# Kernel tuning notes

Hardware: AMD Instinct MI355X
Metric: run time of the kernel (lower is better)

## Reference

```python
import jax, jax.numpy as jnp
import numpy as np

NUM_QRYS = 300
NUM_CLASSES = 80
NUM_PAIRS = 4_000_000
NMS_CANDIDATES = 1000
NMS_THR = 0.65
MAX_SEGS = 100
REFINED_WEIGHT = 2.0
FH = FW = 256  # final mask grid resolution


def setup_inputs() -> dict:
    key = jax.random.key(0)
    k1, k2, k3, k4, k5, k6, k7 = jax.random.split(key, 7)
    cls_logits = jax.random.normal(k1, (NUM_QRYS, NUM_CLASSES + 1), jnp.float32)
    # valid xyxy boxes in normalized [0,1] coords
    b = jax.random.uniform(k2, (NUM_QRYS, 4), jnp.float32)
    x1 = b[:, 0] * 0.7
    y1 = b[:, 1] * 0.7
    x2 = x1 + 0.05 + b[:, 2] * 0.25
    y2 = y1 + 0.05 + b[:, 3] * 0.25
    pred_boxes = jnp.stack([x1, y1, x2, y2], axis=1)
    seg_logits = jax.random.normal(k3, (NUM_PAIRS,), jnp.float32)
    key_xy = jax.random.uniform(k4, (NUM_PAIRS, 2), jnp.float32)
    qry_ids = jax.random.randint(k5, (NUM_PAIRS,), 0, NUM_QRYS, jnp.int32)
    refined_mask = jax.random.randint(k6, (NUM_PAIRS,), 0, 2, jnp.int32).astype(bool)
    map_ids = jax.random.randint(k7, (NUM_PAIRS,), 0, 4, jnp.int32)
    return {"cls_logits": cls_logits, "pred_boxes": pred_boxes, "seg_logits": seg_logits,
            "key_xy": key_xy, "qry_ids": qry_ids, "refined_mask": refined_mask, "map_ids": map_ids}


def _box_iou(boxes):  # boxes: [C,4] xyxy -> [C,C]
    x1 = jnp.maximum(boxes[:, None, 0], boxes[None, :, 0])
    y1 = jnp.maximum(boxes[:, None, 1], boxes[None, :, 1])
    x2 = jnp.minimum(boxes[:, None, 2], boxes[None, :, 2])
    y2 = jnp.minimum(boxes[:, None, 3], boxes[None, :, 3])
    inter = jnp.clip(x2 - x1, 0.0) * jnp.clip(y2 - y1, 0.0)
    area = (boxes[:, 2] - boxes[:, 0]) * (boxes[:, 3] - boxes[:, 1])
    union = area[:, None] + area[None, :] - inter
    return inter / jnp.maximum(union, 1e-9)


def _nms_keep(iou, thr):
    # greedy NMS over score-sorted candidates (rows already in descending score order)
    C = iou.shape[0]
    idx = jnp.arange(C)
    def body(i, keep):
        sup = (iou[i] > thr) & (idx > i) & keep[i]
        return keep & ~sup
    return jax.lax.fori_loop(0, C, body, jnp.ones(C, dtype=bool))


def reference(cls_logits, pred_boxes, seg_logits, key_xy, qry_ids, refined_mask, map_ids):
    num_qrys = cls_logits.shape[0]
    # expand per-query class scores -> flat predictions (batch_size = 1)
    scores = jax.nn.sigmoid(cls_logits[:, :-1]).reshape(-1)          # [Q*C]
    feat_ids = jnp.repeat(jnp.arange(num_qrys), NUM_CLASSES)          # [Q*C]
    labels = jnp.tile(jnp.arange(NUM_CLASSES), num_qrys)              # [Q*C]
    # top-k candidates before NMS
    top_scores, cand = jax.lax.top_k(scores, NMS_CANDIDATES)
    cand_feats = feat_ids[cand]
    cand_labels = labels[cand]
    # class-aware (batched) NMS: offset boxes per label so classes don't suppress each other
    offs = cand_labels.astype(pred_boxes.dtype)[:, None] * 4.0
    cand_boxes = pred_boxes[cand_feats] + offs
    keep = _nms_keep(_box_iou(cand_boxes), NMS_THR)
    kept_scores = jnp.where(keep, top_scores, -jnp.inf)
    sel_scores, sel = jax.lax.top_k(kept_scores, MAX_SEGS)
    sel_scores = jnp.where(jnp.isfinite(sel_scores), sel_scores, 0.0)
    sel_feats = cand_feats[sel]
    # assemble per-query mask logit maps from sparse query-key pairs (scatter-max)
    px = jnp.clip((key_xy[:, 0] * FW).astype(jnp.int32), 0, FW - 1)
    py = jnp.clip((key_xy[:, 1] * FH).astype(jnp.int32), 0, FH - 1)
    w_logits = jnp.where(refined_mask, REFINED_WEIGHT * seg_logits, seg_logits)
    flat = qry_ids * (FH * FW) + py * FW + px                          # [num_pairs]
    qry_maps = jnp.full((num_qrys * FH * FW,), -1e4, cls_logits.dtype).at[flat].max(w_logits)
    qry_maps = qry_maps.reshape(num_qrys, FH, FW)
    mask_probs = jax.nn.sigmoid(qry_maps[sel_feats])                   # [MAX_SEGS, FH, FW]
    # score-weighted soft masks (float output; thresholding at mask_thr yields bool masks)
    return sel_scores[:, None, None] * mask_probs
```

## Files before the change

### kernel.cpp

```cpp
#include <hip/hip_runtime.h>

#define NQ        300
#define NC        80
#define NE        24000
#define CAND      1000
#define KSEL      100
#define NPAIRS    4000000
#define HB        4096
#define FHW       65536
#define NMS_THR_F 0.65f
#define MAPS_INIT 0x39E3BFFFu
#define INIT_VEC4 1638400

__device__ __forceinline__ unsigned enc_f32(float f) {
    unsigned u = __float_as_uint(f);
    return (u & 0x80000000u) ? ~u : (u | 0x80000000u);
}
__device__ __forceinline__ float dec_f32(unsigned k) {
    unsigned u = (k & 0x80000000u) ? (k ^ 0x80000000u) : ~k;
    return __uint_as_float(u);
}

__global__ __launch_bounds__(1024) void k_front(
    const float* __restrict__ cls,
    const float* __restrict__ pboxes,
    const unsigned* __restrict__ refined_raw,
    uint4* __restrict__ maps4,
    float* __restrict__ sel_score_g, int* __restrict__ sel_slot_g,
    int* __restrict__ qry2slot_g, unsigned* __restrict__ mode_flag_g)
{
    if (blockIdx.x > 0) {
        uint4 v; v.x = v.y = v.z = v.w = MAPS_INIT;
        for (int i = (int)(blockIdx.x - 1) * 1024 + (int)threadIdx.x;
             i < INIT_VEC4; i += 256 * 1024)
            maps4[i] = v;
        return;
    }

    __shared__ unsigned long long sbuf[4096];
    __shared__ float sbx[CAND], sby[CAND], sbz[CAND], sbw[CAND];
    __shared__ float sscore[CAND];
    __shared__ short sfeat[CAND];
    __shared__ unsigned char slab[CAND];
    __shared__ unsigned char skeep[CAND];
    __shared__ int wlist[16][64];
    __shared__ int q2s[NQ];
    __shared__ float ss[KSEL]; __shared__ int sf[KSEL];
    __shared__ unsigned subhist[64];
    __shared__ unsigned smode;
    __shared__ int sB, sT, sAbove, sCount, sN;

    unsigned* hist = (unsigned*)sbuf;
    int tid = threadIdx.x;
    int lane = tid & 63, wv = tid >> 6;

    for (int b = tid; b < HB; b += 1024) hist[b] = 0u;
    if (tid < 64) subhist[tid] = 0u;
    if (tid == 0) { smode = 0u; sCount = 0; }
    __syncthreads();

    unsigned long long lk[24];
    #pragma unroll
    for (int k = 0; k < 24; k++) {
        int e = tid + (k << 10);
        if (e < NE) {
            int q = e / NC, c = e - q * NC;
            float x = cls[q * (NC + 1) + c];
            float s = 1.f / (1.f + expf(-x));
            unsigned bits = __float_as_uint(s);
            lk[k] = ((unsigned long long)bits << 32) | (unsigned)(0xFFFFFFFFu - (unsigned)e);
            atomicAdd(&hist[bits >> 18], 1u);
        }
    }
    if (refined_raw[tid] > 1u) atomicOr(&smode, 1u);
    __syncthreads();

    if (tid == 0) {
        int acc = 0, B = 0;
        for (int b = HB - 1; b >= 0; b--) {
            acc += (int)hist[b];
            if (acc >= CAND) { B = b; break; }
        }
        sB = B; sAbove = acc - (int)hist[B];
    }
    __syncthreads();
    unsigned B = (unsigned)sB;

    #pragma unroll
    for (int k = 0; k < 24; k++) {
        int e = tid + (k << 10);
        if (e < NE && (unsigned)(lk[k] >> 50) == B)
            atomicAdd(&subhist[(unsigned)(lk[k] >> 44) & 63u], 1u);
    }
    __syncthreads();
    if (tid == 0) {
        int acc2 = sAbove, T = 0;
        for (int t = 63; t >= 0; t--) {
            acc2 += (int)subhist[t];
            if (acc2 >= CAND) { T = t; break; }
        }
        sT = T; sN = acc2;
    }
    __syncthreads();
    unsigned T = (unsigned)sT;

    #pragma unroll
    for (int k = 0; k < 24; k++) {
        int e = tid + (k << 10);
        if (e < NE) {
            unsigned long long key = lk[k];
            unsigned bkt = (unsigned)(key >> 50);
            unsigned sub = (unsigned)(key >> 44) & 63u;
            if (bkt > B || (bkt == B && sub >= T)) {
                int pos = atomicAdd(&sCount, 1);
                if (pos < 4096) sbuf[pos] = key;
            }
        }
    }
    __syncthreads();
    int n = min(sN, 4096);

    if (n <= 1024) {
        unsigned long long r = (tid < n) ? sbuf[tid] : 0ULL;
        for (int k = 2; k <= 1024; k <<= 1) {
            for (int j = k >> 1; j > 0; j >>= 1) {
                unsigned long long p;
                if (j >= 64) {
                    sbuf[tid] = r; __syncthreads();
                    p = sbuf[tid ^ j]; __syncthreads();
                } else {
                    p = __shfl_xor(r, j, 64);
                }
                bool d = (tid & k) != 0, lower = (tid & j) == 0;
                r = (d != lower) ? (r > p ? r : p) : (r < p ? r : p);
            }
        }
        sbuf[tid] = r;
        __syncthreads();
    } else {
        int nsort = 2048; while (nsort < n) nsort <<= 1;
        for (int i = n + tid; i < nsort; i += 1024) sbuf[i] = 0ULL;
        __syncthreads();
        for (int k = 2; k <= nsort; k <<= 1)
            for (int j = k >> 1; j > 0; j >>= 1) {
                for (int i = tid; i < nsort; i += 1024) {
                    int ixj = i ^ j;
                    if (ixj > i) {
                        unsigned long long a = sbuf[i], b2 = sbuf[ixj];
                        bool up = ((i & k) == 0);
                        if (up ? (a < b2) : (a > b2)) { sbuf[i] = b2; sbuf[ixj] = a; }
                    }
                }
                __syncthreads();
            }
    }

    if (tid < CAND) {
        unsigned long long key = sbuf[tid];
        unsigned bits = (unsigned)(key >> 32);
        unsigned e = 0xFFFFFFFFu - (unsigned)(key & 0xFFFFFFFFu);
        int feat = (int)e / NC, lab = (int)e - feat * NC;
        sscore[tid] = __uint_as_float(bits);
        sfeat[tid]  = (short)feat;
        slab[tid]   = (unsigned char)lab;
        float off = 4.f * (float)lab;
        const float4 pb = ((const float4*)pboxes)[feat];
        sbx[tid] = pb.x + off; sby[tid] = pb.y + off;
        sbz[tid] = pb.z + off; sbw[tid] = pb.w + off;
    }
    __syncthreads();

    for (int li = 0; li < 5; li++) {
        int lab = wv + (li << 4);
        int nb = 0;
        for (int c = 0; c < CAND; c += 64) {
            int i = c + lane;
            bool m = (i < CAND) && ((int)slab[i] == lab);
            unsigned long long bal = __ballot(m);
            if (m) {
                int r = nb + __popcll(bal & ((1ULL << lane) - 1ULL));
                if (r < 64) wlist[wv][r] = i;
            }
            nb += __popcll(bal);
        }
        int nl = min(nb, 64);
        __syncthreads();

        bool alive = lane < nl;
        float bxv = 0.f, byv = 0.f, bzv = 0.f, bwv = 0.f, ar = 0.f;
        int idx = -1;
        if (alive) {
            idx = wlist[wv][lane];
            bxv = sbx[idx]; byv = sby[idx]; bzv = sbz[idx]; bwv = sbw[idx];
            ar = (bzv - bxv) * (bwv - byv);
        }
        bool keep = alive;
        for (int i = 0; i < nl; i++) {
            float bix = __shfl(bxv, i), biy = __shfl(byv, i);
            float biz = __shfl(bzv, i), biw = __shfl(bwv, i);
            float ai  = __shfl(ar, i);
            int   ki  = __shfl((int)keep, i);
            if (ki && keep && lane > i) {
                float xx1 = fmaxf(bix, bxv), yy1 = fmaxf(biy, byv);
                float xx2 = fminf(biz, bzv), yy2 = fminf(biw, bwv);
                float inter = fmaxf(xx2 - xx1, 0.f) * fmaxf(yy2 - yy1, 0.f);
                float uni = ai + ar - inter;
                if (inter / fmaxf(uni, 1e-9f) > NMS_THR_F) keep = false;
            }
        }
        if (alive) skeep[idx] = keep ? 1 : 0;
    }
    __syncthreads();

    for (int q = tid; q < NQ; q += 1024) q2s[q] = -1;
    __syncthreads();
    if (tid < 64) {
        int base = 0;
        for (int c = 0; c < CAND; c += 64) {
            int i = c + lane;
            bool k = (i < CAND) && skeep[i];
            unsigned long long bal = __ballot(k);
            int pos = base + __popcll(bal & ((1ULL << lane) - 1ULL));
            if (k && pos < KSEL) { ss[pos] = sscore[i]; sf[pos] = (int)sfeat[i]; }
            base += __popcll(bal);
        }
        if (tid == 0) {
            int nsel = min(base, KSEL), nslots = 0;
            for (int s = 0; s < KSEL; s++) {
                if (s < nsel) {
                    int f = sf[s];
                    int sl = q2s[f];
                    if (sl < 0) { sl = nslots++; q2s[f] = sl; }
                    sel_slot_g[s] = sl; sel_score_g[s] = ss[s];
                } else {
                    sel_slot_g[s] = -1; sel_score_g[s] = 0.f;
                }
            }
            *mode_flag_g = smode;
        }
    }
    __syncthreads();
    for (int q = tid; q < NQ; q += 1024) qry2slot_g[q] = q2s[q];
}

__global__ __launch_bounds__(256) void k_scatter(
    const float* __restrict__ seg, const float2* __restrict__ xy,
    const int* __restrict__ qry, const unsigned* __restrict__ refined_raw,
    const int* __restrict__ qry2slot, const unsigned* __restrict__ mode_flag,
    unsigned* __restrict__ maps)
{
    int t = blockIdx.x * 256 + threadIdx.x;
    if ((t << 2) >= NPAIRS) return;

    int4 q4 = ((const int4*)qry)[t];
    int s0 = qry2slot[q4.x], s1 = qry2slot[q4.y];
    int s2 = qry2slot[q4.z], s3 = qry2slot[q4.w];
    if ((s0 & s1 & s2 & s3) < 0) return;

    float4 sg   = ((const float4*)seg)[t];
    float4 xy01 = ((const float4*)xy)[2 * t];
    float4 xy23 = ((const float4*)xy)[2 * t + 1];
    unsigned r0, r1, r2, r3;
    if (*mode_flag) {
        unsigned rb = refined_raw[t];
        r0 = rb & 255u; r1 = (rb >> 8) & 255u; r2 = (rb >> 16) & 255u; r3 = rb >> 24;
    } else {
        uint4 rr = ((const uint4*)refined_raw)[t];
        r0 = rr.x; r1 = rr.y; r2 = rr.z; r3 = rr.w;
    }

    #define DO_PAIR(S, PX, PY, W, R)                                              \
        if (S >= 0) {                                                             \
            int px = min(max((int)((PX) * 256.f), 0), 255);                       \
            int py = min(max((int)((PY) * 256.f), 0), 255);                       \
            float w = (R) ? 2.f * (W) : (W);                                      \
            atomicMax(&maps[S * FHW + py * 256 + px], enc_f32(w));                \
        }
    DO_PAIR(s0, xy01.x, xy01.y, sg.x, r0)
    DO_PAIR(s1, xy01.z, xy01.w, sg.y, r1)
    DO_PAIR(s2, xy23.x, xy23.y, sg.z, r2)
    DO_PAIR(s3, xy23.z, xy23.w, sg.w, r3)
    #undef DO_PAIR
}

__global__ __launch_bounds__(256) void k_output(
    const uint4* __restrict__ maps4,
    const float* __restrict__ sel_score, const int* __restrict__ sel_slot,
    float4* __restrict__ out4)
{
    int i = blockIdx.x * 256 + threadIdx.x;
    int s = i >> 14;
    float sc = sel_score[s];
    int slot = sel_slot[s];
    float4 v = {0.f, 0.f, 0.f, 0.f};
    if (slot >= 0) {
        uint4 m = maps4[slot * (FHW / 4) + (i & 16383)];
        v.x = sc / (1.f + expf(-dec_f32(m.x)));
        v.y = sc / (1.f + expf(-dec_f32(m.y)));
        v.z = sc / (1.f + expf(-dec_f32(m.z)));
        v.w = sc / (1.f + expf(-dec_f32(m.w)));
    }
    out4[i] = v;
}

extern "C" void kernel_launch(void* const* d_in, const int* in_sizes, int n_in,
                              void* d_out, int out_size, void* d_ws, size_t ws_size,
                              hipStream_t stream) {
    const float*    cls     = (const float*)d_in[0];
    const float*    pboxes  = (const float*)d_in[1];
    const float*    seg     = (const float*)d_in[2];
    const float2*   xy      = (const float2*)d_in[3];
    const int*      qry     = (const int*)d_in[4];
    const unsigned* refined = (const unsigned*)d_in[5];
    float* out = (float*)d_out;

    char* ws = (char*)d_ws;
    unsigned*  maps      = (unsigned*)ws;
    float*     sel_score = (float*)   (ws + 26214400);
    int*       sel_slot  = (int*)     (ws + 26214800);
    int*       qry2slot  = (int*)     (ws + 26215200);
    unsigned*  mode_flag = (unsigned*)(ws + 26216400);

    k_front  <<<257, 1024, 0, stream>>>(cls, pboxes, refined, (uint4*)maps,
                                        sel_score, sel_slot, qry2slot, mode_flag);
    k_scatter<<<3907, 256, 0, stream>>>(seg, xy, qry, refined, qry2slot, mode_flag, maps);
    k_output <<<6400, 256, 0, stream>>>((const uint4*)maps, sel_score, sel_slot,
                                        (float4*)out);
}
```

Measured before the change: 251.4 us.

## Parallelize top-k threshold scans and slot assignment; spill keys to global scratch

Replaces the single-thread histogram threshold scans with wave-wide shuffle prefix sums and ballots, and replaces the serial per-selection slot assignment loop with a parallel first-occurrence search across one wavefront. The 24 per-thread 64-bit keys are now stored in the output buffer as scratch instead of registers, which frees registers in the 1024-thread block but adds global round-trips. In the scatter kernel the early-exit test on all-negative slots is removed, and the slot lookups are moved after the vector loads so those loads can issue earlier. The removal means every thread now loads all its inputs even when none of its pairs maps to a selected query.

```diff
diff --git a/kernel.cpp b/kernel.cpp
--- a/kernel.cpp
+++ b/kernel.cpp
@@ -12,6 +12,8 @@
 #define MAPS_INIT 0x39E3BFFFu
 #define INIT_VEC4 1638400
 
+typedef unsigned long long ull;
+
 __device__ __forceinline__ unsigned enc_f32(float f) {
     unsigned u = __float_as_uint(f);
     return (u & 0x80000000u) ? ~u : (u | 0x80000000u);
@@ -25,7 +27,7 @@
     const float* __restrict__ cls,
     const float* __restrict__ pboxes,
     const unsigned* __restrict__ refined_raw,
-    uint4* __restrict__ maps4,
+    uint4* __restrict__ maps4, ull* __restrict__ keys_g,
     float* __restrict__ sel_score_g, int* __restrict__ sel_slot_g,
     int* __restrict__ qry2slot_g, unsigned* __restrict__ mode_flag_g)
 {
@@ -37,7 +39,7 @@
         return;
     }
 
-    __shared__ unsigned long long sbuf[4096];
+    __shared__ ull sbuf[4096];
     __shared__ float sbx[CAND], sby[CAND], sbz[CAND], sbw[CAND];
     __shared__ float sscore[CAND];
     __shared__ short sfeat[CAND];
@@ -56,10 +58,9 @@
 
     for (int b = tid; b < HB; b += 1024) hist[b] = 0u;
     if (tid < 64) subhist[tid] = 0u;
-    if (tid == 0) { smode = 0u; sCount = 0; }
-    __syncthreads();
-
-    unsigned long long lk[24];
+    if (tid == 0) { smode = 0u; sCount = 0; sB = 0; sAbove = 0; }
+    __syncthreads();
+
     #pragma unroll
     for (int k = 0; k < 24; k++) {
         int e = tid + (k << 10);
@@ -68,47 +69,69 @@
             float x = cls[q * (NC + 1) + c];
             float s = 1.f / (1.f + expf(-x));
             unsigned bits = __float_as_uint(s);
-            lk[k] = ((unsigned long long)bits << 32) | (unsigned)(0xFFFFFFFFu - (unsigned)e);
+            keys_g[e] = ((ull)bits << 32) | (unsigned)(0xFFFFFFFFu - (unsigned)e);
             atomicAdd(&hist[bits >> 18], 1u);
         }
     }
     if (refined_raw[tid] > 1u) atomicOr(&smode, 1u);
     __syncthreads();
 
-    if (tid == 0) {
-        int acc = 0, B = 0;
-        for (int b = HB - 1; b >= 0; b--) {
-            acc += (int)hist[b];
-            if (acc >= CAND) { B = b; break; }
-        }
-        sB = B; sAbove = acc - (int)hist[B];
+    if (tid < 64) {
+        int acc = 0;
+        for (int base = HB - 64; base >= 0; base -= 64) {
+            unsigned h = hist[base + lane];
+            unsigned r = h;
+            #pragma unroll
+            for (int d = 1; d < 64; d <<= 1) {
+                unsigned t2 = __shfl_down(r, d, 64);
+                if (lane + d < 64) r += t2;
+            }
+            ull m = __ballot(acc + (int)r >= CAND);
+            if (m) {
+                int hi = 63 - __clzll(m);
+                int rB = __shfl((int)r, hi, 64);
+                int hB = __shfl((int)h, hi, 64);
+                if (lane == 0) { sB = base + hi; sAbove = acc + rB - hB; }
+                break;
+            }
+            acc += __shfl((int)r, 0, 64);
+        }
     }
     __syncthreads();
     unsigned B = (unsigned)sB;
-
-    #pragma unroll
-    for (int k = 0; k < 24; k++) {
-        int e = tid + (k << 10);
-        if (e < NE && (unsigned)(lk[k] >> 50) == B)
-            atomicAdd(&subhist[(unsigned)(lk[k] >> 44) & 63u], 1u);
-    }
-    __syncthreads();
-    if (tid == 0) {
-        int acc2 = sAbove, T = 0;
-        for (int t = 63; t >= 0; t--) {
-            acc2 += (int)subhist[t];
-            if (acc2 >= CAND) { T = t; break; }
-        }
-        sT = T; sN = acc2;
-    }
-    __syncthreads();
-    unsigned T = (unsigned)sT;
 
     #pragma unroll
     for (int k = 0; k < 24; k++) {
         int e = tid + (k << 10);
         if (e < NE) {
-            unsigned long long key = lk[k];
+            ull key = keys_g[e];
+            if ((unsigned)(key >> 50) == B)
+                atomicAdd(&subhist[(unsigned)(key >> 44) & 63u], 1u);
+        }
+    }
+    __syncthreads();
+    if (tid < 64) {
+        unsigned h = subhist[lane];
+        unsigned r = h;
+        #pragma unroll
+        for (int d = 1; d < 64; d <<= 1) {
+            unsigned t2 = __shfl_down(r, d, 64);
+            if (lane + d < 64) r += t2;
+        }
+        int above = sAbove;
+        ull m = __ballot(above + (int)r >= CAND);
+        int hi = 63 - __clzll(m);
+        int rT = __shfl((int)r, hi, 64);
+        if (lane == 0) { sT = hi; sN = above + rT; }
+    }
+    __syncthreads();
+    unsigned T = (unsigned)sT;
+
+    #pragma unroll
+    for (int k = 0; k < 24; k++) {
+        int e = tid + (k << 10);
+        if (e < NE) {
+            ull key = keys_g[e];
             unsigned bkt = (unsigned)(key >> 50);
             unsigned sub = (unsigned)(key >> 44) & 63u;
             if (bkt > B || (bkt == B && sub >= T)) {
@@ -121,10 +144,10 @@
     int n = min(sN, 4096);
 
     if (n <= 1024) {
-        unsigned long long r = (tid < n) ? sbuf[tid] : 0ULL;
+        ull r = (tid < n) ? sbuf[tid] : 0ULL;
         for (int k = 2; k <= 1024; k <<= 1) {
             for (int j = k >> 1; j > 0; j >>= 1) {
-                unsigned long long p;
+                ull p;
                 if (j >= 64) {
                     sbuf[tid] = r; __syncthreads();
                     p = sbuf[tid ^ j]; __syncthreads();
@@ -146,7 +169,7 @@
                 for (int i = tid; i < nsort; i += 1024) {
                     int ixj = i ^ j;
                     if (ixj > i) {
-                        unsigned long long a = sbuf[i], b2 = sbuf[ixj];
+                        ull a = sbuf[i], b2 = sbuf[ixj];
                         bool up = ((i & k) == 0);
                         if (up ? (a < b2) : (a > b2)) { sbuf[i] = b2; sbuf[ixj] = a; }
                     }
@@ -156,7 +179,7 @@
     }
 
     if (tid < CAND) {
-        unsigned long long key = sbuf[tid];
+        ull key = sbuf[tid];
         unsigned bits = (unsigned)(key >> 32);
         unsigned e = 0xFFFFFFFFu - (unsigned)(key & 0xFFFFFFFFu);
         int feat = (int)e / NC, lab = (int)e - feat * NC;
@@ -176,7 +199,7 @@
         for (int c = 0; c < CAND; c += 64) {
             int i = c + lane;
             bool m = (i < CAND) && ((int)slab[i] == lab);
-            unsigned long long bal = __ballot(m);
+            ull bal = __ballot(m);
             if (m) {
                 int r = nb + __popcll(bal & ((1ULL << lane) - 1ULL));
                 if (r < 64) wlist[wv][r] = i;
@@ -218,26 +241,35 @@
         int base = 0;
         for (int c = 0; c < CAND; c += 64) {
             int i = c + lane;
-            bool k = (i < CAND) && skeep[i];
-            unsigned long long bal = __ballot(k);
+            bool k2 = (i < CAND) && skeep[i];
+            ull bal = __ballot(k2);
             int pos = base + __popcll(bal & ((1ULL << lane) - 1ULL));
-            if (k && pos < KSEL) { ss[pos] = sscore[i]; sf[pos] = (int)sfeat[i]; }
+            if (k2 && pos < KSEL) { ss[pos] = sscore[i]; sf[pos] = (int)sfeat[i]; }
             base += __popcll(bal);
         }
-        if (tid == 0) {
-            int nsel = min(base, KSEL), nslots = 0;
-            for (int s = 0; s < KSEL; s++) {
-                if (s < nsel) {
-                    int f = sf[s];
-                    int sl = q2s[f];
-                    if (sl < 0) { sl = nslots++; q2s[f] = sl; }
-                    sel_slot_g[s] = sl; sel_score_g[s] = ss[s];
-                } else {
-                    sel_slot_g[s] = -1; sel_score_g[s] = 0.f;
-                }
-            }
-            *mode_flag_g = smode;
-        }
+        int nsel = min(base, KSEL);
+        int s1 = lane, s2 = lane + 64;
+        int fp1 = s1, fp2 = s2;
+        if (s1 < nsel) { int f = sf[s1]; for (int k2 = 0; k2 < s1; k2++) if (sf[k2] == f) { fp1 = k2; break; } }
+        if (s2 < nsel) { int f = sf[s2]; for (int k2 = 0; k2 < s2; k2++) if (sf[k2] == f) { fp2 = k2; break; } }
+        bool fo1 = (s1 < nsel) && (fp1 == s1);
+        bool fo2 = (s2 < nsel) && (fp2 == s2);
+        ull b1 = __ballot(fo1);
+        ull b2 = __ballot(fo2);
+        int c1 = __popcll(b1);
+        int slot1 = -1, slot2 = -1;
+        if (s1 < nsel) slot1 = __popcll(b1 & ((1ULL << fp1) - 1ULL));
+        if (s2 < nsel) slot2 = (fp2 < 64) ? __popcll(b1 & ((1ULL << fp2) - 1ULL))
+                                          : c1 + __popcll(b2 & ((1ULL << (fp2 - 64)) - 1ULL));
+        sel_slot_g[s1] = slot1;
+        sel_score_g[s1] = (s1 < nsel) ? ss[s1] : 0.f;
+        if (s2 < KSEL) {
+            sel_slot_g[s2] = slot2;
+            sel_score_g[s2] = (s2 < nsel) ? ss[s2] : 0.f;
+        }
+        if (fo1) q2s[sf[s1]] = slot1;
+        if (fo2) q2s[sf[s2]] = slot2;
+        if (lane == 0) *mode_flag_g = smode;
     }
     __syncthreads();
     for (int q = tid; q < NQ; q += 1024) qry2slot_g[q] = q2s[q];
@@ -252,11 +284,7 @@
     int t = blockIdx.x * 256 + threadIdx.x;
     if ((t << 2) >= NPAIRS) return;
 
-    int4 q4 = ((const int4*)qry)[t];
-    int s0 = qry2slot[q4.x], s1 = qry2slot[q4.y];
-    int s2 = qry2slot[q4.z], s3 = qry2slot[q4.w];
-    if ((s0 & s1 & s2 & s3) < 0) return;
-
+    int4 q4     = ((const int4*)qry)[t];
     float4 sg   = ((const float4*)seg)[t];
     float4 xy01 = ((const float4*)xy)[2 * t];
     float4 xy23 = ((const float4*)xy)[2 * t + 1];
@@ -268,6 +296,8 @@
         uint4 rr = ((const uint4*)refined_raw)[t];
         r0 = rr.x; r1 = rr.y; r2 = rr.z; r3 = rr.w;
     }
+    int s0 = qry2slot[q4.x], s1 = qry2slot[q4.y];
+    int s2 = qry2slot[q4.z], s3 = qry2slot[q4.w];
 
     #define DO_PAIR(S, PX, PY, W, R)                                              \
         if (S >= 0) {                                                             \
@@ -320,8 +350,9 @@
     int*       sel_slot  = (int*)     (ws + 26214800);
     int*       qry2slot  = (int*)     (ws + 26215200);
     unsigned*  mode_flag = (unsigned*)(ws + 26216400);
-
-    k_front  <<<257, 1024, 0, stream>>>(cls, pboxes, refined, (uint4*)maps,
+    ull*       keys      = (ull*)d_out;
+
+    k_front  <<<257, 1024, 0, stream>>>(cls, pboxes, refined, (uint4*)maps, keys,
                                         sel_score, sel_slot, qry2slot, mode_flag);
     k_scatter<<<3907, 256, 0, stream>>>(seg, xy, qry, refined, qry2slot, mode_flag, maps);
     k_output <<<6400, 256, 0, stream>>>((const uint4*)maps, sel_score, sel_slot,
```

Result: no change. 253.4 us (+0.8%).
